# Optimization experiments

Hardware: AMD Instinct MI355X
Metric: run time of the kernel (lower is better)

Reference implementation:

```python
import jax, jax.numpy as jnp
import numpy as np

# norse default LIF/LI parameters
DT = 0.001
TAU_SYN_INV = 200.0
TAU_MEM_INV = 100.0
V_TH = 1.0
ALPHA = 100.0        # SuperSpike surrogate slope (method='super', alpha=100)
T_ENC = 40           # ConstantCurrentLIFEncoder(40)
SCALE = 50.0

STATE_DIM = 256
ACTIONS = 18
HIDDEN = 128
BATCH = 1024

@jax.custom_vjp
def spike(x):
    return (x > 0).astype(x.dtype)

def _spike_fwd(x):
    return spike(x), x

def _spike_bwd(x, g):
    # SuperSpike surrogate: 1 / (alpha*|x| + 1)^2
    return (g / (ALPHA * jnp.abs(x) + 1.0) ** 2,)

spike.defvjp(_spike_fwd, _spike_bwd)

def encode(current):
    # constant-current LIF encoder: current [B, D] -> spikes [T_ENC, B, D]
    def step(v, _):
        v = v + DT * TAU_MEM_INV * (-v + current)   # v_leak = 0
        z = spike(v - V_TH)
        v = (1.0 - z) * v                            # reset to v_reset = 0
        return v, z
    _, zs = jax.lax.scan(step, jnp.zeros_like(current), None, length=T_ENC)
    return zs

def snn_forward(x, w_in, w_rec, w_actor, w_critic):
    # encode positive and negative rectified currents, concat on feature dim
    xs = jnp.concatenate([encode(jax.nn.relu(SCALE * x)),
                          encode(jax.nn.relu(-SCALE * x))], axis=2)  # [T, B, 2D]
    B = x.shape[0]
    H = w_in.shape[0]
    A = w_actor.shape[0]
    dt_ = x.dtype
    carry0 = (jnp.zeros((B, H), dt_), jnp.zeros((B, H), dt_), jnp.zeros((B, H), dt_),
              jnp.zeros((B, A), dt_), jnp.zeros((B, A), dt_),
              jnp.zeros((B, 1), dt_), jnp.zeros((B, 1), dt_))

    def step(carry, x_t):
        z, v, i, va, ia, vc, ic = carry
        # --- recurrent LIFCell (norse lif_step) ---
        v_dec = v + DT * TAU_MEM_INV * (-v + i)      # dv uses pre-decay i
        i_dec = i - DT * TAU_SYN_INV * i
        z_new = spike(v_dec - V_TH)
        v_new = (1.0 - z_new) * v_dec                # reset by z to v_reset = 0
        i_new = i_dec + x_t @ w_in.T + z @ w_rec.T   # recurrent input uses old z
        # --- LICell actor readout (norse li_step) ---
        va_new = va + DT * TAU_MEM_INV * (-va + ia)
        ia_new = ia - DT * TAU_SYN_INV * ia + z_new @ w_actor.T
        # --- LICell critic readout ---
        vc_new = vc + DT * TAU_MEM_INV * (-vc + ic)
        ic_new = ic - DT * TAU_SYN_INV * ic + z_new @ w_critic.T
        return (z_new, v_new, i_new, va_new, ia_new, vc_new, ic_new), (va_new, vc_new)

    _, (volt_a, volt_c) = jax.lax.scan(step, carry0, xs)
    m_a = jnp.max(volt_a, axis=0)                    # max over time
    m_c = jnp.max(volt_c, axis=0)
    return jax.nn.softmax(m_a, axis=1), m_c


def setup_inputs() -> dict:
    key = jax.random.key(0)
    k0, k1, k2, k3, k4 = jax.random.split(key, 5)
    in_feat = 2 * STATE_DIM
    x = jax.random.normal(k0, (BATCH, STATE_DIM), dtype=jnp.float32)
    # norse init: randn * sqrt(2 / input_size)
    w_in = jax.random.normal(k1, (HIDDEN, in_feat), dtype=jnp.float32) * np.sqrt(2.0 / in_feat)
    w_rec = jax.random.normal(k2, (HIDDEN, HIDDEN), dtype=jnp.float32) * np.sqrt(2.0 / HIDDEN)
    w_actor = jax.random.normal(k3, (ACTIONS, HIDDEN), dtype=jnp.float32) * np.sqrt(2.0 / HIDDEN)
    w_critic = jax.random.normal(k4, (1, HIDDEN), dtype=jnp.float32) * np.sqrt(2.0 / HIDDEN)
    return {"x": x, "w_in": w_in, "w_rec": w_rec, "w_actor": w_actor, "w_critic": w_critic}


def reference(x, w_in, w_rec, w_actor, w_critic):
    return snn_forward(x, w_in, w_rec, w_actor, w_critic)
```

## Files before the change

kernel.cpp:

```cpp
#include <hip/hip_runtime.h>
#include <hip/hip_bf16.h>
#include <stdint.h>

typedef __attribute__((ext_vector_type(4))) float f32x4;
typedef __attribute__((ext_vector_type(8))) short s16x8;
typedef __attribute__((ext_vector_type(4))) unsigned int u32x4;

#define OFF_WHI  2621440
#define OFF_WLO  2752512
#define OFF_WAHI 3014656
#define OFF_WALO 3022848
#define OFF_I    3031040
#define OFF_ZB   24002560

__device__ __forceinline__ void lut_entry(uint32_t by, uint32_t* r) {
    uint32_t r0 = 0, r1 = 0, r2 = 0, r3 = 0;
    if (by & 1)   r0 |= 0x3F80u;
    if (by & 2)   r0 |= 0x3F800000u;
    if (by & 4)   r1 |= 0x3F80u;
    if (by & 8)   r1 |= 0x3F800000u;
    if (by & 16)  r2 |= 0x3F80u;
    if (by & 32)  r2 |= 0x3F800000u;
    if (by & 64)  r3 |= 0x3F80u;
    if (by & 128) r3 |= 0x3F800000u;
    r[0] = r0; r[1] = r1; r[2] = r2; r[3] = r3;
}

__global__ __launch_bounds__(256) void k_prep_enc(const float* __restrict__ x,
                                                  const float* __restrict__ w_in,
                                                  const float* __restrict__ w_actor,
                                                  const float* __restrict__ w_critic,
                                                  uint32_t* __restrict__ spk,
                                                  __hip_bfloat16* __restrict__ whi,
                                                  __hip_bfloat16* __restrict__ wlo,
                                                  __hip_bfloat16* __restrict__ wahi,
                                                  __hip_bfloat16* __restrict__ walo) {
    const int bid = blockIdx.x;
    if (bid < 2048) {
        int gid  = bid * 256 + threadIdx.x;
        int b    = gid >> 9;
        int f    = gid & 511;
        int lane = threadIdx.x & 63;
        float xv  = x[b * 256 + (f & 255)];
        float cur = (f < 256) ? fmaxf(50.f * xv, 0.f) : fmaxf(-50.f * xv, 0.f);
        int wbase = (f >> 6) << 1;
        float v = 0.f;
        for (int t = 0; t < 40; ++t) {
            v = v + 0.1f * (cur - v);
            bool z = (v - 1.0f) > 0.f;
            unsigned long long m = __ballot(z);
            if (z) v = 0.f;
            if (lane == 0)
                *(unsigned long long*)&spk[(size_t)(t * 1024 + b) * 16 + wbase] = m;
        }
    } else {
        int i = (bid - 2048) * 256 + threadIdx.x;
        float w = w_in[i];
        __hip_bfloat16 h = __float2bfloat16(w);
        whi[i] = h;
        wlo[i] = __float2bfloat16(w - __bfloat162float(h));
        if (i < 4096) {
            int a = i >> 7, j = i & 127;
            float v = (a < 18) ? w_actor[a * 128 + j] : ((a == 18) ? w_critic[j] : 0.f);
            __hip_bfloat16 vh = __float2bfloat16(v);
            wahi[i] = vh;
            walo[i] = __float2bfloat16(v - __bfloat162float(vh));
        }
    }
}

__global__ __launch_bounds__(512, 1) void k_ingemm(const uint32_t* __restrict__ spk,
                                                   const __hip_bfloat16* __restrict__ whi,
                                                   const __hip_bfloat16* __restrict__ wlo,
                                                   float* __restrict__ I) {
    __shared__ uint32_t lut[256][4];
    __shared__ float tile[16][128];
    const int tid = threadIdx.x;
    if (tid < 256) lut_entry(tid, lut[tid]);
    const int lane = tid & 63, wid = tid >> 6;
    const int fr = lane & 15, fo = lane >> 4;
    const int n0 = wid * 16;

#define LOADB(i) s16x8 bh##i, bl##i; { int off = (n0 + fr) * 512 + (i) * 32 + fo * 8; \
    bh##i = *(const s16x8*)(whi + off); bl##i = *(const s16x8*)(wlo + off); }
    LOADB(0)  LOADB(1)  LOADB(2)  LOADB(3)  LOADB(4)  LOADB(5)  LOADB(6)  LOADB(7)
    LOADB(8)  LOADB(9)  LOADB(10) LOADB(11) LOADB(12) LOADB(13) LOADB(14) LOADB(15)
#undef LOADB
    asm volatile("" : "+v"(bh0), "+v"(bh1), "+v"(bh2),  "+v"(bh3),
                      "+v"(bh4), "+v"(bh5), "+v"(bh6),  "+v"(bh7),
                      "+v"(bh8), "+v"(bh9), "+v"(bh10), "+v"(bh11),
                      "+v"(bh12),"+v"(bh13),"+v"(bh14), "+v"(bh15));
    asm volatile("" : "+v"(bl0), "+v"(bl1), "+v"(bl2),  "+v"(bl3),
                      "+v"(bl4), "+v"(bl5), "+v"(bl6),  "+v"(bl7),
                      "+v"(bl8), "+v"(bl9), "+v"(bl10), "+v"(bl11),
                      "+v"(bl12),"+v"(bl13),"+v"(bl14), "+v"(bl15));
    __syncthreads();

    const int m0 = blockIdx.x * 160;
    const int srow = tid >> 5;
    const int sc0  = (tid & 31) * 4;
    for (int mt = 0; mt < 10; ++mt) {
        int mrow = m0 + mt * 16 + fr;
        u32x4 w0 = *(const u32x4*)&spk[mrow * 16];
        u32x4 w1 = *(const u32x4*)&spk[mrow * 16 + 4];
        u32x4 w2 = *(const u32x4*)&spk[mrow * 16 + 8];
        u32x4 w3 = *(const u32x4*)&spk[mrow * 16 + 12];
        f32x4 acc = (f32x4)0.f;
#define KSTEP(i, WSEL) { uint32_t by = ((WSEL) >> (fo * 8)) & 0xFFu; \
        union { u32x4 u; s16x8 v; } cv; cv.u = *(const u32x4*)lut[by]; \
        acc = __builtin_amdgcn_mfma_f32_16x16x32_bf16(cv.v, bh##i, acc, 0, 0, 0); \
        acc = __builtin_amdgcn_mfma_f32_16x16x32_bf16(cv.v, bl##i, acc, 0, 0, 0); }
        KSTEP(0,  w0[0]) KSTEP(1,  w0[1]) KSTEP(2,  w0[2]) KSTEP(3,  w0[3])
        KSTEP(4,  w1[0]) KSTEP(5,  w1[1]) KSTEP(6,  w1[2]) KSTEP(7,  w1[3])
        KSTEP(8,  w2[0]) KSTEP(9,  w2[1]) KSTEP(10, w2[2]) KSTEP(11, w2[3])
        KSTEP(12, w3[0]) KSTEP(13, w3[1]) KSTEP(14, w3[2]) KSTEP(15, w3[3])
#undef KSTEP
        __syncthreads();
#pragma unroll
        for (int r = 0; r < 4; ++r)
            tile[fo * 4 + r][n0 + fr] = acc[r];
        __syncthreads();
        f32x4 vv = *(const f32x4*)&tile[srow][sc0];
        *(f32x4*)&I[(size_t)(m0 + mt * 16 + srow) * 128 + sc0] = vv;
    }
}

__global__ __launch_bounds__(256, 1) void k_recur(const float* __restrict__ I,
                                                  const float* __restrict__ w_rec,
                                                  unsigned long long* __restrict__ zbits) {
    __shared__ uint32_t lut[256][4];
    __shared__ uint32_t zm[2][16][4];
    const int tid = threadIdx.x;
    lut_entry(tid, lut[tid]);
    if (tid < 64) zm[0][tid >> 2][tid & 3] = 0;
    const int lane = tid & 63, w = tid >> 6;
    const int fr = lane & 15, fo = lane >> 4;
    const int n0 = w * 32;
    const int b0 = blockIdx.x * 16;
    uint32_t* zb32 = (uint32_t*)zbits;

#define LOADW(ks, ni) s16x8 H##ks##ni, L##ks##ni, Q##ks##ni; { \
    const float* p = w_rec + (n0 + (ni) * 16 + fr) * 128 + (ks) * 32 + fo * 8; \
    _Pragma("unroll") for (int j = 0; j < 8; ++j) { \
        float f = p[j]; \
        __hip_bfloat16 hb = __float2bfloat16(f); \
        float r1 = f - __bfloat162float(hb); \
        __hip_bfloat16 lb = __float2bfloat16(r1); \
        float r2 = r1 - __bfloat162float(lb); \
        __hip_bfloat16 qb = __float2bfloat16(r2); \
        H##ks##ni[j] = (short)*(unsigned short*)&hb; \
        L##ks##ni[j] = (short)*(unsigned short*)&lb; \
        Q##ks##ni[j] = (short)*(unsigned short*)&qb; } }
    LOADW(0,0) LOADW(1,0) LOADW(2,0) LOADW(3,0)
    LOADW(0,1) LOADW(1,1) LOADW(2,1) LOADW(3,1)
#undef LOADW
    asm volatile("" : "+v"(H00), "+v"(H10), "+v"(H20), "+v"(H30),
                      "+v"(H01), "+v"(H11), "+v"(H21), "+v"(H31),
                      "+v"(L00), "+v"(L10), "+v"(L20), "+v"(L30));
    asm volatile("" : "+v"(L01), "+v"(L11), "+v"(L21), "+v"(L31),
                      "+v"(Q00), "+v"(Q10), "+v"(Q20), "+v"(Q30),
                      "+v"(Q01), "+v"(Q11), "+v"(Q21), "+v"(Q31));

    f32x4 v0 = (f32x4)0.f, v1 = (f32x4)0.f, c0 = (f32x4)0.f, c1 = (f32x4)0.f;

#define ILOAD(dst, t_, ni) { _Pragma("unroll") for (int r = 0; r < 4; ++r) \
    dst[r] = I[(size_t)((t_) * 1024 + b0 + fo * 4 + r) * 128 + n0 + (ni) * 16 + fr]; }
    f32x4 icur0, icur1;
    ILOAD(icur0, 0, 0) ILOAD(icur1, 0, 1)
    __syncthreads();

    for (int t = 0; t < 40; ++t) {
        int tn = (t < 39) ? t + 1 : 39;
        f32x4 inxt0, inxt1;
        ILOAD(inxt0, tn, 0) ILOAD(inxt1, tn, 1)

        u32x4 zw = *(const u32x4*)zm[t & 1][fr];
        union { u32x4 u; s16x8 v; } a0, a1, a2, a3;
        a0.u = *(const u32x4*)lut[(zw[0] >> (fo * 8)) & 0xFFu];
        a1.u = *(const u32x4*)lut[(zw[1] >> (fo * 8)) & 0xFFu];
        a2.u = *(const u32x4*)lut[(zw[2] >> (fo * 8)) & 0xFFu];
        a3.u = *(const u32x4*)lut[(zw[3] >> (fo * 8)) & 0xFFu];

        f32x4 r0 = (f32x4)0.f, r1 = (f32x4)0.f;
#define RECK(ks, av) \
        r0 = __builtin_amdgcn_mfma_f32_16x16x32_bf16(av, H##ks##0, r0, 0, 0, 0); \
        r0 = __builtin_amdgcn_mfma_f32_16x16x32_bf16(av, L##ks##0, r0, 0, 0, 0); \
        r0 = __builtin_amdgcn_mfma_f32_16x16x32_bf16(av, Q##ks##0, r0, 0, 0, 0); \
        r1 = __builtin_amdgcn_mfma_f32_16x16x32_bf16(av, H##ks##1, r1, 0, 0, 0); \
        r1 = __builtin_amdgcn_mfma_f32_16x16x32_bf16(av, L##ks##1, r1, 0, 0, 0); \
        r1 = __builtin_amdgcn_mfma_f32_16x16x32_bf16(av, Q##ks##1, r1, 0, 0, 0);
        RECK(0, a0.v) RECK(1, a1.v) RECK(2, a2.v) RECK(3, a3.v)
#undef RECK

        f32x4 vd0 = v0 + 0.1f * (c0 - v0);
        f32x4 vd1 = v1 + 0.1f * (c1 - v1);
        f32x4 id0 = c0 - 0.2f * c0;
        f32x4 id1 = c1 - 0.2f * c1;
        unsigned long long B00, B01, B02, B03, B10, B11, B12, B13;
        bool z;
        z = (vd0[0] - 1.0f) > 0.f; B00 = __ballot(z); if (z) vd0[0] = 0.f;
        z = (vd0[1] - 1.0f) > 0.f; B01 = __ballot(z); if (z) vd0[1] = 0.f;
        z = (vd0[2] - 1.0f) > 0.f; B02 = __ballot(z); if (z) vd0[2] = 0.f;
        z = (vd0[3] - 1.0f) > 0.f; B03 = __ballot(z); if (z) vd0[3] = 0.f;
        z = (vd1[0] - 1.0f) > 0.f; B10 = __ballot(z); if (z) vd1[0] = 0.f;
        z = (vd1[1] - 1.0f) > 0.f; B11 = __ballot(z); if (z) vd1[1] = 0.f;
        z = (vd1[2] - 1.0f) > 0.f; B12 = __ballot(z); if (z) vd1[2] = 0.f;
        z = (vd1[3] - 1.0f) > 0.f; B13 = __ballot(z); if (z) vd1[3] = 0.f;
        v0 = vd0; v1 = vd1;

        if (lane < 16) {
            int m = lane, rq = m & 3, sh = (m >> 2) * 16;
            unsigned long long s0 = (rq == 0) ? B00 : (rq == 1) ? B01 : (rq == 2) ? B02 : B03;
            unsigned long long s1 = (rq == 0) ? B10 : (rq == 1) ? B11 : (rq == 2) ? B12 : B13;
            uint32_t word = ((uint32_t)(s0 >> sh) & 0xFFFFu)
                          | (((uint32_t)(s1 >> sh) & 0xFFFFu) << 16);
            zm[(t & 1) ^ 1][m][w] = word;
            zb32[((size_t)t * 1024 + b0 + m) * 4 + w] = word;
        }

        c0 = (id0 + icur0) + r0;
        c1 = (id1 + icur1) + r1;
        icur0 = inxt0; icur1 = inxt1;
        __syncthreads();
    }
#undef ILOAD
}

__global__ __launch_bounds__(64) void k_readout(const uint32_t* __restrict__ zb,
                                                const __hip_bfloat16* __restrict__ wahi,
                                                const __hip_bfloat16* __restrict__ walo,
                                                float* __restrict__ out) {
    __shared__ uint32_t lut[256][4];
    const int lane = threadIdx.x;
    for (int i0 = lane; i0 < 256; i0 += 64) lut_entry(i0, lut[i0]);
    const int fr = lane & 15, fo = lane >> 4;
    const int b0 = blockIdx.x * 16;

    s16x8 bf[2][4][2];
#pragma unroll
    for (int ni = 0; ni < 2; ++ni)
#pragma unroll
        for (int ks = 0; ks < 4; ++ks) {
            int off = (ni * 16 + fr) * 128 + ks * 32 + fo * 8;
            bf[ni][ks][0] = *(const s16x8*)(wahi + off);
            bf[ni][ks][1] = *(const s16x8*)(walo + off);
        }
    __syncthreads();

    f32x4 va[2], ia[2], ma_[2];
#pragma unroll
    for (int ni = 0; ni < 2; ++ni) {
        va[ni] = (f32x4)0.f; ia[ni] = (f32x4)0.f; ma_[ni] = (f32x4)(-1e30f);
    }

    for (int t = 0; t < 40; ++t) {
        int m = t * 1024 + b0 + fr;
        u32x4 zw = *(const u32x4*)&zb[(size_t)m * 4];
        f32x4 acc[2];
        acc[0] = (f32x4)0.f; acc[1] = (f32x4)0.f;
#pragma unroll
        for (int ks = 0; ks < 4; ++ks) {
            uint32_t by = (zw[ks] >> (fo * 8)) & 0xFFu;
            union { u32x4 u; s16x8 v; } cv;
            cv.u = *(const u32x4*)lut[by];
            s16x8 af = cv.v;
            acc[0] = __builtin_amdgcn_mfma_f32_16x16x32_bf16(af, bf[0][ks][0], acc[0], 0, 0, 0);
            acc[0] = __builtin_amdgcn_mfma_f32_16x16x32_bf16(af, bf[0][ks][1], acc[0], 0, 0, 0);
            acc[1] = __builtin_amdgcn_mfma_f32_16x16x32_bf16(af, bf[1][ks][0], acc[1], 0, 0, 0);
            acc[1] = __builtin_amdgcn_mfma_f32_16x16x32_bf16(af, bf[1][ks][1], acc[1], 0, 0, 0);
        }
#pragma unroll
        for (int ni = 0; ni < 2; ++ni) {
            f32x4 nva = va[ni] + 0.1f * (ia[ni] - va[ni]);
            ia[ni] = ia[ni] - 0.2f * ia[ni] + acc[ni];
            va[ni] = nva;
#pragma unroll
            for (int r = 0; r < 4; ++r)
                ma_[ni][r] = fmaxf(ma_[ni][r], nva[r]);
        }
    }

#pragma unroll
    for (int r = 0; r < 4; ++r) {
        int b = b0 + fo * 4 + r;
        float x0 = ma_[0][r];
        float x1 = (fr < 2) ? ma_[1][r] : -1e30f;
        float mx = fmaxf(x0, x1);
#pragma unroll
        for (int d = 1; d < 16; d <<= 1) mx = fmaxf(mx, __shfl_xor(mx, d));
        float e0 = expf(x0 - mx);
        float e1 = (fr < 2) ? expf(ma_[1][r] - mx) : 0.f;
        float s = e0 + e1;
#pragma unroll
        for (int d = 1; d < 16; d <<= 1) s += __shfl_xor(s, d);
        out[b * 18 + fr] = e0 / s;
        if (fr < 2) out[b * 18 + 16 + fr] = e1 / s;
        if (fr == 2) out[18432 + b] = ma_[1][r];
    }
}

extern "C" void kernel_launch(void* const* d_in, const int* in_sizes, int n_in,
                              void* d_out, int out_size, void* d_ws, size_t ws_size,
                              hipStream_t stream) {
    const float* x        = (const float*)d_in[0];
    const float* w_in     = (const float*)d_in[1];
    const float* w_rec    = (const float*)d_in[2];
    const float* w_actor  = (const float*)d_in[3];
    const float* w_critic = (const float*)d_in[4];
    float* out = (float*)d_out;
    char* ws = (char*)d_ws;
    uint32_t*           spk  = (uint32_t*)ws;
    __hip_bfloat16*     whi  = (__hip_bfloat16*)(ws + OFF_WHI);
    __hip_bfloat16*     wlo  = (__hip_bfloat16*)(ws + OFF_WLO);
    __hip_bfloat16*     wahi = (__hip_bfloat16*)(ws + OFF_WAHI);
    __hip_bfloat16*     walo = (__hip_bfloat16*)(ws + OFF_WALO);
    float*              I    = (float*)(ws + OFF_I);
    unsigned long long* zb   = (unsigned long long*)(ws + OFF_ZB);

    hipLaunchKernelGGL(k_prep_enc, dim3(2304), dim3(256), 0, stream,
                       x, w_in, w_actor, w_critic, spk, whi, wlo, wahi, walo);
    hipLaunchKernelGGL(k_ingemm,   dim3(256),  dim3(512), 0, stream, spk, whi, wlo, I);
    hipLaunchKernelGGL(k_recur,    dim3(64),   dim3(256), 0, stream, I, w_rec, zb);
    hipLaunchKernelGGL(k_readout,  dim3(64),   dim3(64),  0, stream,
                       (const uint32_t*)zb, wahi, walo, out);
}
```

Measured before the change: 152.2 us.

## Fuse readout into recurrent kernel and split weights inside consumer kernels

The actor/critic readout is folded into the recurrent kernel: two waves run the readout MFMAs on the shared-memory spike bits each timestep, and softmax is done at the end through shared memory. This removes the global z-bit buffer and a separate readout launch. The bf16 hi/lo splitting of w_in and of the readout weights now happens inside the consuming kernels rather than in the prep kernel, so the prep kernel only encodes. The cost is extra per-step work on the recurrent critical path and redundant weight conversion in every block.

```diff
diff --git a/kernel.cpp b/kernel.cpp
--- a/kernel.cpp
+++ b/kernel.cpp
@@ -6,12 +6,7 @@
 typedef __attribute__((ext_vector_type(8))) short s16x8;
 typedef __attribute__((ext_vector_type(4))) unsigned int u32x4;
 
-#define OFF_WHI  2621440
-#define OFF_WLO  2752512
-#define OFF_WAHI 3014656
-#define OFF_WALO 3022848
-#define OFF_I    3031040
-#define OFF_ZB   24002560
+#define OFF_I 2621440
 
 __device__ __forceinline__ void lut_entry(uint32_t by, uint32_t* r) {
     uint32_t r0 = 0, r1 = 0, r2 = 0, r3 = 0;
@@ -26,52 +21,28 @@
     r[0] = r0; r[1] = r1; r[2] = r2; r[3] = r3;
 }
 
-__global__ __launch_bounds__(256) void k_prep_enc(const float* __restrict__ x,
-                                                  const float* __restrict__ w_in,
-                                                  const float* __restrict__ w_actor,
-                                                  const float* __restrict__ w_critic,
-                                                  uint32_t* __restrict__ spk,
-                                                  __hip_bfloat16* __restrict__ whi,
-                                                  __hip_bfloat16* __restrict__ wlo,
-                                                  __hip_bfloat16* __restrict__ wahi,
-                                                  __hip_bfloat16* __restrict__ walo) {
-    const int bid = blockIdx.x;
-    if (bid < 2048) {
-        int gid  = bid * 256 + threadIdx.x;
-        int b    = gid >> 9;
-        int f    = gid & 511;
-        int lane = threadIdx.x & 63;
-        float xv  = x[b * 256 + (f & 255)];
-        float cur = (f < 256) ? fmaxf(50.f * xv, 0.f) : fmaxf(-50.f * xv, 0.f);
-        int wbase = (f >> 6) << 1;
-        float v = 0.f;
-        for (int t = 0; t < 40; ++t) {
-            v = v + 0.1f * (cur - v);
-            bool z = (v - 1.0f) > 0.f;
-            unsigned long long m = __ballot(z);
-            if (z) v = 0.f;
-            if (lane == 0)
-                *(unsigned long long*)&spk[(size_t)(t * 1024 + b) * 16 + wbase] = m;
-        }
-    } else {
-        int i = (bid - 2048) * 256 + threadIdx.x;
-        float w = w_in[i];
-        __hip_bfloat16 h = __float2bfloat16(w);
-        whi[i] = h;
-        wlo[i] = __float2bfloat16(w - __bfloat162float(h));
-        if (i < 4096) {
-            int a = i >> 7, j = i & 127;
-            float v = (a < 18) ? w_actor[a * 128 + j] : ((a == 18) ? w_critic[j] : 0.f);
-            __hip_bfloat16 vh = __float2bfloat16(v);
-            wahi[i] = vh;
-            walo[i] = __float2bfloat16(v - __bfloat162float(vh));
-        }
+__global__ __launch_bounds__(256) void k_encode(const float* __restrict__ x,
+                                                uint32_t* __restrict__ spk) {
+    int gid  = blockIdx.x * 256 + threadIdx.x;
+    int b    = gid >> 9;
+    int f    = gid & 511;
+    int lane = threadIdx.x & 63;
+    float xv  = x[b * 256 + (f & 255)];
+    float cur = (f < 256) ? fmaxf(50.f * xv, 0.f) : fmaxf(-50.f * xv, 0.f);
+    int wbase = (f >> 6) << 1;
+    float v = 0.f;
+    for (int t = 0; t < 40; ++t) {
+        v = v + 0.1f * (cur - v);
+        bool z = (v - 1.0f) > 0.f;
+        unsigned long long m = __ballot(z);
+        if (z) v = 0.f;
+        if (lane == 0)
+            *(unsigned long long*)&spk[(size_t)(t * 1024 + b) * 16 + wbase] = m;
     }
 }
 
 __global__ __launch_bounds__(512, 1) void k_ingemm(const uint32_t* __restrict__ spk,
-                                                   const __hip_bfloat16* __restrict__ whi,
-                                                   const __hip_bfloat16* __restrict__ wlo,
+                                                   const float* __restrict__ w_in,
                                                    float* __restrict__ I) {
     __shared__ uint32_t lut[256][4];
     __shared__ float tile[16][128];
@@ -81,8 +52,16 @@
     const int fr = lane & 15, fo = lane >> 4;
     const int n0 = wid * 16;
 
-#define LOADB(i) s16x8 bh##i, bl##i; { int off = (n0 + fr) * 512 + (i) * 32 + fo * 8; \
-    bh##i = *(const s16x8*)(whi + off); bl##i = *(const s16x8*)(wlo + off); }
+#define LOADB(i) s16x8 bh##i, bl##i; { \
+    const float* p = w_in + (n0 + fr) * 512 + (i) * 32 + fo * 8; \
+    f32x4 fa = *(const f32x4*)p; f32x4 fb = *(const f32x4*)(p + 4); \
+    _Pragma("unroll") for (int j = 0; j < 8; ++j) { \
+        float f = (j < 4) ? fa[j] : fb[j - 4]; \
+        __hip_bfloat16 hb = __float2bfloat16(f); \
+        float r1 = f - __bfloat162float(hb); \
+        __hip_bfloat16 lb = __float2bfloat16(r1); \
+        bh##i[j] = (short)*(unsigned short*)&hb; \
+        bl##i[j] = (short)*(unsigned short*)&lb; } }
     LOADB(0)  LOADB(1)  LOADB(2)  LOADB(3)  LOADB(4)  LOADB(5)  LOADB(6)  LOADB(7)
     LOADB(8)  LOADB(9)  LOADB(10) LOADB(11) LOADB(12) LOADB(13) LOADB(14) LOADB(15)
 #undef LOADB
@@ -125,11 +104,14 @@
     }
 }
 
-__global__ __launch_bounds__(256, 1) void k_recur(const float* __restrict__ I,
-                                                  const float* __restrict__ w_rec,
-                                                  unsigned long long* __restrict__ zbits) {
+__global__ __launch_bounds__(256, 1) void k_recur_ro(const float* __restrict__ I,
+                                                     const float* __restrict__ w_rec,
+                                                     const float* __restrict__ w_actor,
+                                                     const float* __restrict__ w_critic,
+                                                     float* __restrict__ out) {
     __shared__ uint32_t lut[256][4];
     __shared__ uint32_t zm[2][16][4];
+    __shared__ float smax[16][20];
     const int tid = threadIdx.x;
     lut_entry(tid, lut[tid]);
     if (tid < 64) zm[0][tid >> 2][tid & 3] = 0;
@@ -137,7 +119,6 @@
     const int fr = lane & 15, fo = lane >> 4;
     const int n0 = w * 32;
     const int b0 = blockIdx.x * 16;
-    uint32_t* zb32 = (uint32_t*)zbits;
 
 #define LOADW(ks, ni) s16x8 H##ks##ni, L##ks##ni, Q##ks##ni; { \
     const float* p = w_rec + (n0 + (ni) * 16 + fr) * 128 + (ks) * 32 + fo * 8; \
@@ -161,6 +142,24 @@
                       "+v"(Q00), "+v"(Q10), "+v"(Q20), "+v"(Q30),
                       "+v"(Q01), "+v"(Q11), "+v"(Q21), "+v"(Q31));
 
+    s16x8 rbh[4], rbl[4];
+    const int a_ch = w * 16 + fr;
+    const float* asrc = (a_ch < 18) ? (w_actor + a_ch * 128)
+                       : ((a_ch == 18) ? w_critic : nullptr);
+#pragma unroll
+    for (int ks = 0; ks < 4; ++ks) {
+#pragma unroll
+        for (int j = 0; j < 8; ++j) {
+            float f = asrc ? asrc[ks * 32 + fo * 8 + j] : 0.f;
+            __hip_bfloat16 hb = __float2bfloat16(f);
+            float r1 = f - __bfloat162float(hb);
+            __hip_bfloat16 lb = __float2bfloat16(r1);
+            rbh[ks][j] = (short)*(unsigned short*)&hb;
+            rbl[ks][j] = (short)*(unsigned short*)&lb;
+        }
+    }
+    f32x4 rva = (f32x4)0.f, ria = (f32x4)0.f, rma = (f32x4)(-1e30f);
+
     f32x4 v0 = (f32x4)0.f, v1 = (f32x4)0.f, c0 = (f32x4)0.f, c1 = (f32x4)0.f;
 
 #define ILOAD(dst, t_, ni) { _Pragma("unroll") for (int r = 0; r < 4; ++r) \
@@ -215,87 +214,54 @@
             uint32_t word = ((uint32_t)(s0 >> sh) & 0xFFFFu)
                           | (((uint32_t)(s1 >> sh) & 0xFFFFu) << 16);
             zm[(t & 1) ^ 1][m][w] = word;
-            zb32[((size_t)t * 1024 + b0 + m) * 4 + w] = word;
         }
 
         c0 = (id0 + icur0) + r0;
         c1 = (id1 + icur1) + r1;
         icur0 = inxt0; icur1 = inxt1;
         __syncthreads();
+
+        if (w < 2) {
+            u32x4 zw2 = *(const u32x4*)zm[(t & 1) ^ 1][fr];
+            f32x4 racc = (f32x4)0.f;
+#pragma unroll
+            for (int ks = 0; ks < 4; ++ks) {
+                uint32_t by = (zw2[ks] >> (fo * 8)) & 0xFFu;
+                union { u32x4 u; s16x8 v; } cv;
+                cv.u = *(const u32x4*)lut[by];
+                racc = __builtin_amdgcn_mfma_f32_16x16x32_bf16(cv.v, rbh[ks], racc, 0, 0, 0);
+                racc = __builtin_amdgcn_mfma_f32_16x16x32_bf16(cv.v, rbl[ks], racc, 0, 0, 0);
+            }
+            f32x4 nva = rva + 0.1f * (ria - rva);
+            ria = ria - 0.2f * ria + racc;
+            rva = nva;
+#pragma unroll
+            for (int r = 0; r < 4; ++r)
+                rma[r] = fmaxf(rma[r], nva[r]);
+        }
     }
 #undef ILOAD
-}
-
-__global__ __launch_bounds__(64) void k_readout(const uint32_t* __restrict__ zb,
-                                                const __hip_bfloat16* __restrict__ wahi,
-                                                const __hip_bfloat16* __restrict__ walo,
-                                                float* __restrict__ out) {
-    __shared__ uint32_t lut[256][4];
-    const int lane = threadIdx.x;
-    for (int i0 = lane; i0 < 256; i0 += 64) lut_entry(i0, lut[i0]);
-    const int fr = lane & 15, fo = lane >> 4;
-    const int b0 = blockIdx.x * 16;
-
-    s16x8 bf[2][4][2];
-#pragma unroll
-    for (int ni = 0; ni < 2; ++ni)
-#pragma unroll
-        for (int ks = 0; ks < 4; ++ks) {
-            int off = (ni * 16 + fr) * 128 + ks * 32 + fo * 8;
-            bf[ni][ks][0] = *(const s16x8*)(wahi + off);
-            bf[ni][ks][1] = *(const s16x8*)(walo + off);
-        }
+
+    if (w == 0) {
+#pragma unroll
+        for (int r = 0; r < 4; ++r) smax[fo * 4 + r][fr] = rma[r];
+    } else if (w == 1 && fr < 3) {
+#pragma unroll
+        for (int r = 0; r < 4; ++r) smax[fo * 4 + r][16 + fr] = rma[r];
+    }
     __syncthreads();
-
-    f32x4 va[2], ia[2], ma_[2];
-#pragma unroll
-    for (int ni = 0; ni < 2; ++ni) {
-        va[ni] = (f32x4)0.f; ia[ni] = (f32x4)0.f; ma_[ni] = (f32x4)(-1e30f);
-    }
-
-    for (int t = 0; t < 40; ++t) {
-        int m = t * 1024 + b0 + fr;
-        u32x4 zw = *(const u32x4*)&zb[(size_t)m * 4];
-        f32x4 acc[2];
-        acc[0] = (f32x4)0.f; acc[1] = (f32x4)0.f;
-#pragma unroll
-        for (int ks = 0; ks < 4; ++ks) {
-            uint32_t by = (zw[ks] >> (fo * 8)) & 0xFFu;
-            union { u32x4 u; s16x8 v; } cv;
-            cv.u = *(const u32x4*)lut[by];
-            s16x8 af = cv.v;
-            acc[0] = __builtin_amdgcn_mfma_f32_16x16x32_bf16(af, bf[0][ks][0], acc[0], 0, 0, 0);
-            acc[0] = __builtin_amdgcn_mfma_f32_16x16x32_bf16(af, bf[0][ks][1], acc[0], 0, 0, 0);
-            acc[1] = __builtin_amdgcn_mfma_f32_16x16x32_bf16(af, bf[1][ks][0], acc[1], 0, 0, 0);
-            acc[1] = __builtin_amdgcn_mfma_f32_16x16x32_bf16(af, bf[1][ks][1], acc[1], 0, 0, 0);
-        }
-#pragma unroll
-        for (int ni = 0; ni < 2; ++ni) {
-            f32x4 nva = va[ni] + 0.1f * (ia[ni] - va[ni]);
-            ia[ni] = ia[ni] - 0.2f * ia[ni] + acc[ni];
-            va[ni] = nva;
-#pragma unroll
-            for (int r = 0; r < 4; ++r)
-                ma_[ni][r] = fmaxf(ma_[ni][r], nva[r]);
-        }
-    }
-
-#pragma unroll
-    for (int r = 0; r < 4; ++r) {
-        int b = b0 + fo * 4 + r;
-        float x0 = ma_[0][r];
-        float x1 = (fr < 2) ? ma_[1][r] : -1e30f;
-        float mx = fmaxf(x0, x1);
-#pragma unroll
-        for (int d = 1; d < 16; d <<= 1) mx = fmaxf(mx, __shfl_xor(mx, d));
-        float e0 = expf(x0 - mx);
-        float e1 = (fr < 2) ? expf(ma_[1][r] - mx) : 0.f;
-        float s = e0 + e1;
-#pragma unroll
-        for (int d = 1; d < 16; d <<= 1) s += __shfl_xor(s, d);
-        out[b * 18 + fr] = e0 / s;
-        if (fr < 2) out[b * 18 + 16 + fr] = e1 / s;
-        if (fr == 2) out[18432 + b] = ma_[1][r];
+    if (tid < 16) {
+        int row = tid;
+        float mx = -1e30f;
+#pragma unroll
+        for (int a2 = 0; a2 < 18; ++a2) mx = fmaxf(mx, smax[row][a2]);
+        float s = 0.f;
+#pragma unroll
+        for (int a2 = 0; a2 < 18; ++a2) s += expf(smax[row][a2] - mx);
+#pragma unroll
+        for (int a2 = 0; a2 < 18; ++a2)
+            out[(b0 + row) * 18 + a2] = expf(smax[row][a2] - mx) / s;
+        out[18432 + b0 + row] = smax[row][18];
     }
 }
 
@@ -309,18 +275,11 @@
     const float* w_critic = (const float*)d_in[4];
     float* out = (float*)d_out;
     char* ws = (char*)d_ws;
-    uint32_t*           spk  = (uint32_t*)ws;
-    __hip_bfloat16*     whi  = (__hip_bfloat16*)(ws + OFF_WHI);
-    __hip_bfloat16*     wlo  = (__hip_bfloat16*)(ws + OFF_WLO);
-    __hip_bfloat16*     wahi = (__hip_bfloat16*)(ws + OFF_WAHI);
-    __hip_bfloat16*     walo = (__hip_bfloat16*)(ws + OFF_WALO);
-    float*              I    = (float*)(ws + OFF_I);
-    unsigned long long* zb   = (unsigned long long*)(ws + OFF_ZB);
-
-    hipLaunchKernelGGL(k_prep_enc, dim3(2304), dim3(256), 0, stream,
-                       x, w_in, w_actor, w_critic, spk, whi, wlo, wahi, walo);
-    hipLaunchKernelGGL(k_ingemm,   dim3(256),  dim3(512), 0, stream, spk, whi, wlo, I);
-    hipLaunchKernelGGL(k_recur,    dim3(64),   dim3(256), 0, stream, I, w_rec, zb);
-    hipLaunchKernelGGL(k_readout,  dim3(64),   dim3(64),  0, stream,
-                       (const uint32_t*)zb, wahi, walo, out);
-}
+    uint32_t* spk = (uint32_t*)ws;
+    float*    I   = (float*)(ws + OFF_I);
+
+    hipLaunchKernelGGL(k_encode,   dim3(2048), dim3(256), 0, stream, x, spk);
+    hipLaunchKernelGGL(k_ingemm,   dim3(256),  dim3(512), 0, stream, spk, w_in, I);
+    hipLaunchKernelGGL(k_recur_ro, dim3(64),   dim3(256), 0, stream,
+                       I, w_rec, w_actor, w_critic, out);
+}
```

New measurement: 135.0 us. 1.13x faster.
